# Kernel optimization log

Measured on AMD Instinct MI355X. Metric: run time of the kernel, lower is better.

The kernel has to match this reference:

```python
import jax, jax.numpy as jnp
import numpy as np


def setup_inputs() -> dict:
    key = jax.random.key(0)
    kq, kk, kv = jax.random.split(key, 3)
    N, D = 4096, 1024
    q = jax.random.normal(kq, (N, D), dtype=jnp.float32)
    k = jax.random.normal(kk, (N, D), dtype=jnp.float32)
    v = jax.random.normal(kv, (N, D), dtype=jnp.float32)
    return {"q": q, "k": k, "v": v}


def reference(q, k, v):
    # q, k, v: [N, D]. scale=None, attn_mask unused, dropout p=0.0 (identity).
    scores = jnp.einsum('nd,md->nm', q, k)          # [N, N] logits
    attn = jax.nn.softmax(scores, axis=-1)          # softmax over keys (dim 2 in the [1,N,N] view)
    context = jnp.einsum('nm,md->nd', attn, v)      # [N, D]
    return context
```

## Files before the change

### kernel.cpp

```cpp
#include <hip/hip_runtime.h>
#include <hip/hip_bf16.h>

typedef __attribute__((ext_vector_type(8))) short short8;
typedef __attribute__((ext_vector_type(4))) float float4v;
typedef __attribute__((ext_vector_type(4))) int int4v;

#define L2E 1.44269504088896f
#define SHIFT_C 120.0f
#define QS1 14.0f
#define QS2 3556.0f
#define RATIO 254
#define INV_SS (1.0f / (14.0f * 3556.0f))

#define DRAIN_VM asm volatile("s_waitcnt vmcnt(0)" ::: "memory")
__device__ inline void barrier_raw() {
    asm volatile("" ::: "memory");
    __builtin_amdgcn_s_barrier();
    asm volatile("" ::: "memory");
}

__device__ inline unsigned short f2bf_rne(float x) {
    unsigned int u = __float_as_uint(x);
    u += 0x7FFFu + ((u >> 16) & 1u);
    return (unsigned short)(u >> 16);
}

__device__ inline void gload_lds16(const void* g, void* l) {
    __builtin_amdgcn_global_load_lds(
        (const __attribute__((address_space(1))) void*)g,
        (__attribute__((address_space(3))) void*)l, 16, 0, 0);
}

__global__ __launch_bounds__(256) void prep_fused(
    const float* __restrict__ q, const float* __restrict__ k,
    const float* __restrict__ v,
    signed char* __restrict__ qa, signed char* __restrict__ qb,
    signed char* __restrict__ ka, signed char* __restrict__ kb,
    unsigned short* __restrict__ vt)
{
    __shared__ float tile[32][33];
    int bid = blockIdx.x;
    if (bid < 8192) {
        const size_t n4 = (size_t)4096 * 1024 / 4;
        size_t idx = (size_t)bid * 256 + threadIdx.x;
        const float* src; signed char *da, *db; size_t base;
        if (idx < n4) { src = q; da = qa; db = qb; base = idx; }
        else          { src = k; da = ka; db = kb; base = idx - n4; }
        float4 xv = ((const float4*)src)[base];
        float xs[4] = {xv.x, xv.y, xv.z, xv.w};
        int a[4], b[4];
#pragma unroll
        for (int i = 0; i < 4; ++i) {
            int ia = __float2int_rn(QS1 * xs[i]);
            ia = ia > 127 ? 127 : (ia < -127 ? -127 : ia);
            int ib = __float2int_rn(QS2 * (xs[i] - (float)ia * (1.0f / QS1)));
            ib = ib > 127 ? 127 : (ib < -127 ? -127 : ib);
            a[i] = ia; b[i] = ib;
        }
        unsigned int pa = (a[0] & 255) | ((a[1] & 255) << 8) | ((a[2] & 255) << 16) | ((a[3] & 255) << 24);
        unsigned int pb = (b[0] & 255) | ((b[1] & 255) << 8) | ((b[2] & 255) << 16) | ((b[3] & 255) << 24);
        ((unsigned int*)da)[base] = pa;
        ((unsigned int*)db)[base] = pb;
    } else {
        int b = bid - 8192;
        int k0 = (b & 127) * 32;
        int d0 = (b >> 7) * 32;
        int tx = threadIdx.x & 31, ty = threadIdx.x >> 5;
#pragma unroll
        for (int i = 0; i < 4; ++i) {
            int r = ty + i * 8;
            tile[r][tx] = v[(size_t)(k0 + r) * 1024 + d0 + tx];
        }
        __syncthreads();
#pragma unroll
        for (int i = 0; i < 4; ++i) {
            int r = ty + i * 8;
            vt[(size_t)(d0 + r) * 4096 + k0 + tx] = f2bf_rne(tile[tx][r]);
        }
    }
}

__global__ __launch_bounds__(256) void gemm_qk(
    const signed char* __restrict__ qa, const signed char* __restrict__ qb,
    const signed char* __restrict__ ka, const signed char* __restrict__ kb,
    unsigned short* __restrict__ Pl, float* __restrict__ psum)
{
    __shared__ __align__(16) signed char lds[65536];
    int tid = threadIdx.x;
    int bx = blockIdx.x, by = blockIdx.y;
    int row0 = by * 128, col0 = bx * 128;
    int wave = tid >> 6, lane = tid & 63;
    int wr = (wave >> 1) * 64, wc = (wave & 1) * 64;
    int quad = lane >> 4, lrow = lane & 15;

    int4v acc[4][4];
#pragma unroll
    for (int mi = 0; mi < 4; ++mi)
#pragma unroll
        for (int ni = 0; ni < 4; ++ni) acc[mi][ni] = (int4v){0, 0, 0, 0};

    {
        int sr = lane >> 3, lb = (lane & 7) ^ sr;
        const signed char* gA = qa + (size_t)(row0 + wave * 32 + sr) * 1024 + lb * 16;
        const signed char* gB = ka + (size_t)(col0 + wave * 32 + sr) * 1024 + lb * 16;
        auto stageA = [&](int b, int kc) {
            signed char* lA = lds + b * 32768 + wave * 4096;
            signed char* lB = lds + b * 32768 + 16384 + wave * 4096;
#pragma unroll
            for (int j = 0; j < 4; ++j) {
                gload_lds16(gA + (size_t)j * 8 * 1024 + kc, lA + j * 1024);
                gload_lds16(gB + (size_t)j * 8 * 1024 + kc, lB + j * 1024);
            }
        };
        stageA(0, 0);
        DRAIN_VM; barrier_raw();
        int cur = 0;
        for (int kc = 0; kc < 1024; kc += 128) {
            if (kc + 128 < 1024) stageA(cur ^ 1, kc + 128);
            const signed char* base = lds + cur * 32768;
#pragma unroll
            for (int ks = 0; ks < 2; ++ks) {
                int4v af[4], bf[4];
                int bo = ((ks * 4 + quad) ^ (lrow & 7)) * 16;
#pragma unroll
                for (int mi = 0; mi < 4; ++mi)
                    af[mi] = *(const int4v*)&base[(wr + mi * 16 + lrow) * 128 + bo];
#pragma unroll
                for (int ni = 0; ni < 4; ++ni)
                    bf[ni] = *(const int4v*)&base[16384 + (wc + ni * 16 + lrow) * 128 + bo];
#pragma unroll
                for (int mi = 0; mi < 4; ++mi)
#pragma unroll
                    for (int ni = 0; ni < 4; ++ni)
                        acc[mi][ni] = __builtin_amdgcn_mfma_i32_16x16x64_i8(
                            af[mi], bf[ni], acc[mi][ni], 0, 0, 0);
            }
            DRAIN_VM; barrier_raw();
            cur ^= 1;
        }
    }

#pragma unroll
    for (int mi = 0; mi < 4; ++mi)
#pragma unroll
        for (int ni = 0; ni < 4; ++ni)
#pragma unroll
            for (int r = 0; r < 4; ++r) acc[mi][ni][r] *= RATIO;

    {
        int sr2 = lane >> 2;
        int lb2 = (lane & 3) ^ ((sr2 >> 1) & 3);
        const signed char* gqa = qa + (size_t)(row0 + wave * 32 + sr2) * 1024 + lb2 * 16;
        const signed char* gqb = qb + (size_t)(row0 + wave * 32 + sr2) * 1024 + lb2 * 16;
        const signed char* gka = ka + (size_t)(col0 + wave * 32 + sr2) * 1024 + lb2 * 16;
        const signed char* gkb = kb + (size_t)(col0 + wave * 32 + sr2) * 1024 + lb2 * 16;
        auto stageB = [&](int b, int kc) {
            signed char* base = lds + b * 32768;
#pragma unroll
            for (int j = 0; j < 2; ++j) {
                size_t go = (size_t)j * 16 * 1024 + kc;
                int lo = wave * 2048 + j * 1024;
                gload_lds16(gqa + go, base + lo);
                gload_lds16(gqb + go, base + 8192 + lo);
                gload_lds16(gka + go, base + 16384 + lo);
                gload_lds16(gkb + go, base + 24576 + lo);
            }
        };
        stageB(0, 0);
        DRAIN_VM; barrier_raw();
        int cur = 0;
        for (int kc = 0; kc < 1024; kc += 64) {
            if (kc + 64 < 1024) stageB(cur ^ 1, kc + 64);
            const signed char* base = lds + cur * 32768;
            const signed char* Tqa = base;
            const signed char* Tqb = base + 8192;
            const signed char* Tka = base + 16384;
            const signed char* Tkb = base + 24576;
            int po = (quad ^ ((lrow >> 1) & 3)) * 16;
            {
                int4v fA[4], fB[4];
#pragma unroll
                for (int mi = 0; mi < 4; ++mi)
                    fA[mi] = *(const int4v*)&Tqa[(wr + mi * 16 + lrow) * 64 + po];
#pragma unroll
                for (int ni = 0; ni < 4; ++ni)
                    fB[ni] = *(const int4v*)&Tkb[(wc + ni * 16 + lrow) * 64 + po];
#pragma unroll
                for (int mi = 0; mi < 4; ++mi)
#pragma unroll
                    for (int ni = 0; ni < 4; ++ni)
                        acc[mi][ni] = __builtin_amdgcn_mfma_i32_16x16x64_i8(
                            fA[mi], fB[ni], acc[mi][ni], 0, 0, 0);
            }
            {
                int4v fA[4], fB[4];
#pragma unroll
                for (int mi = 0; mi < 4; ++mi)
                    fA[mi] = *(const int4v*)&Tqb[(wr + mi * 16 + lrow) * 64 + po];
#pragma unroll
                for (int ni = 0; ni < 4; ++ni)
                    fB[ni] = *(const int4v*)&Tka[(wc + ni * 16 + lrow) * 64 + po];
#pragma unroll
                for (int mi = 0; mi < 4; ++mi)
#pragma unroll
                    for (int ni = 0; ni < 4; ++ni)
                        acc[mi][ni] = __builtin_amdgcn_mfma_i32_16x16x64_i8(
                            fA[mi], fB[ni], acc[mi][ni], 0, 0, 0);
            }
            DRAIN_VM; barrier_raw();
            cur ^= 1;
        }
    }

    int strip = bx * 2 + (wave & 1);
#pragma unroll
    for (int mi = 0; mi < 4; ++mi)
#pragma unroll
        for (int r = 0; r < 4; ++r) {
            int row = row0 + wr + mi * 16 + quad * 4 + r;
            float p[4], s = 0.f;
#pragma unroll
            for (int ni = 0; ni < 4; ++ni) {
                float sv = (float)acc[mi][ni][r] * INV_SS;
                p[ni] = exp2f((sv - SHIFT_C) * L2E);
                s += p[ni];
            }
#pragma unroll
            for (int d = 1; d < 16; d <<= 1) s += __shfl_xor(s, d);
#pragma unroll
            for (int ni = 0; ni < 4; ++ni)
                Pl[(size_t)row * 4096 + col0 + wc + ni * 16 + lrow] = f2bf_rne(p[ni]);
            if (lrow == 0) psum[row * 64 + strip] = s;
        }
}

__global__ __launch_bounds__(256) void gemm_pv(
    const unsigned short* __restrict__ P, const unsigned short* __restrict__ vt,
    float* __restrict__ part)
{
    __shared__ __align__(16) unsigned short Ls[32768];
    int tid = threadIdx.x;
    int bx = blockIdx.x, by = blockIdx.y;
    int row0 = by * 128, col0 = bx * 128;
    int kc0 = blockIdx.z * 2048;
    int wave = tid >> 6, lane = tid & 63;
    int wr = (wave >> 1) * 64, wc = (wave & 1) * 64;
    int quad = lane >> 4, lrow = lane & 15;
    int sr = lane >> 3, lb = (lane & 7) ^ sr;
    int swz = lrow & 7;

    float4v acc[4][4];
#pragma unroll
    for (int mi = 0; mi < 4; ++mi)
#pragma unroll
        for (int ni = 0; ni < 4; ++ni) acc[mi][ni] = (float4v){0.f, 0.f, 0.f, 0.f};

    const unsigned short* gA = P  + (size_t)(row0 + wave * 32 + sr) * 4096 + kc0 + lb * 8;
    const unsigned short* gB = vt + (size_t)(col0 + wave * 32 + sr) * 4096 + kc0 + lb * 8;

    auto stage = [&](int b, int kc) {
        unsigned short* lA = Ls + b * 16384 + wave * 2048;
        unsigned short* lB = Ls + b * 16384 + 8192 + wave * 2048;
#pragma unroll
        for (int j = 0; j < 4; ++j) {
            gload_lds16(gA + (size_t)j * 8 * 4096 + kc, lA + j * 512);
            gload_lds16(gB + (size_t)j * 8 * 4096 + kc, lB + j * 512);
        }
    };

    stage(0, 0);
    DRAIN_VM; barrier_raw();
    int cur = 0;
    for (int kc = 0; kc < 2048; kc += 64) {
        if (kc + 64 < 2048) stage(cur ^ 1, kc + 64);
        const unsigned short* As = Ls + cur * 16384;
        const unsigned short* Bs = As + 8192;
#pragma unroll
        for (int ks = 0; ks < 2; ++ks) {
            short8 af[4], bf[4];
            int bo = ((ks * 4 + quad) ^ swz) * 8;
#pragma unroll
            for (int mi = 0; mi < 4; ++mi)
                af[mi] = *(const short8*)&As[(wr + mi * 16 + lrow) * 64 + bo];
#pragma unroll
            for (int ni = 0; ni < 4; ++ni)
                bf[ni] = *(const short8*)&Bs[(wc + ni * 16 + lrow) * 64 + bo];
#pragma unroll
            for (int mi = 0; mi < 4; ++mi)
#pragma unroll
                for (int ni = 0; ni < 4; ++ni)
                    acc[mi][ni] = __builtin_amdgcn_mfma_f32_16x16x32_bf16(
                        af[mi], bf[ni], acc[mi][ni], 0, 0, 0);
        }
        DRAIN_VM; barrier_raw();
        cur ^= 1;
    }
    float* po = part + (size_t)blockIdx.z * 4096 * 1024;
#pragma unroll
    for (int mi = 0; mi < 4; ++mi)
#pragma unroll
        for (int ni = 0; ni < 4; ++ni)
#pragma unroll
            for (int r = 0; r < 4; ++r) {
                int row = row0 + wr + mi * 16 + quad * 4 + r;
                int col = col0 + wc + ni * 16 + lrow;
                po[(size_t)row * 1024 + col] = acc[mi][ni][r];
            }
}

__global__ __launch_bounds__(256) void reduce_out(
    const float* __restrict__ part, const float* __restrict__ psum,
    float* __restrict__ out)
{
    __shared__ float rs;
    int row = blockIdx.x;
    int tid = threadIdx.x;
    if (tid < 64) {
        float s = psum[row * 64 + tid];
#pragma unroll
        for (int d = 1; d < 64; d <<= 1) s += __shfl_xor(s, d);
        if (tid == 0) rs = 1.0f / s;
    }
    __syncthreads();
    float rinv = rs;
    size_t idx = (size_t)row * 256 + tid;
    const float4* p0 = (const float4*)part;
    const float4* p1 = (const float4*)(part + (size_t)4096 * 1024);
    float4 a = p0[idx], b = p1[idx];
    float4 o = {(a.x + b.x) * rinv, (a.y + b.y) * rinv,
                (a.z + b.z) * rinv, (a.w + b.w) * rinv};
    ((float4*)out)[idx] = o;
}

__global__ __launch_bounds__(256) void attn_fallback(
    const float* __restrict__ q, const float* __restrict__ k,
    const float* __restrict__ v, float* __restrict__ out)
{
    __shared__ float qs[1024];
    __shared__ float ps[4096];
    __shared__ float red[256];
    int row = blockIdx.x, tid = threadIdx.x;
    for (int i = tid; i < 1024; i += 256) qs[i] = q[(size_t)row * 1024 + i];
    __syncthreads();
    for (int j = tid; j < 4096; j += 256) {
        const float* kr = &k[(size_t)j * 1024];
        float s = 0.f;
        for (int d = 0; d < 1024; ++d) s += qs[d] * kr[d];
        ps[j] = s;
    }
    __syncthreads();
    float m = -3.4e38f;
    for (int j = tid; j < 4096; j += 256) m = fmaxf(m, ps[j]);
    red[tid] = m; __syncthreads();
    for (int s2 = 128; s2 > 0; s2 >>= 1) {
        if (tid < s2) red[tid] = fmaxf(red[tid], red[tid + s2]);
        __syncthreads();
    }
    m = red[0]; __syncthreads();
    float l = 0.f;
    for (int j = tid; j < 4096; j += 256) {
        float p = exp2f((ps[j] - m) * L2E);
        ps[j] = p; l += p;
    }
    red[tid] = l; __syncthreads();
    for (int s2 = 128; s2 > 0; s2 >>= 1) {
        if (tid < s2) red[tid] += red[tid + s2];
        __syncthreads();
    }
    float rinv = 1.0f / red[0];
    __syncthreads();
    for (int c = tid; c < 1024; c += 256) {
        float o = 0.f;
        for (int j = 0; j < 4096; ++j) o += ps[j] * v[(size_t)j * 1024 + c];
        out[(size_t)row * 1024 + c] = o * rinv;
    }
}

extern "C" void kernel_launch(void* const* d_in, const int* in_sizes, int n_in,
                              void* d_out, int out_size, void* d_ws, size_t ws_size,
                              hipStream_t stream) {
    const float* q = (const float*)d_in[0];
    const float* k = (const float*)d_in[1];
    const float* v = (const float*)d_in[2];
    float* out = (float*)d_out;

    const size_t SZ_P = (size_t)4096 * 4096 * 2;
    const size_t SZ_I = (size_t)4096 * 1024;
    const size_t SZ_H = (size_t)4096 * 1024 * 2;
    const size_t SZ_T = (size_t)4096 * 64 * 4;
    const size_t SZ_PR = (size_t)4096 * 1024 * 4 * 2;
    size_t off = 0;
    char* ws = (char*)d_ws;
    unsigned short* Pbuf = (unsigned short*)(ws + off); off += SZ_P;
    signed char*    qa   = (signed char*)(ws + off);    off += SZ_I;
    signed char*    qb   = (signed char*)(ws + off);    off += SZ_I;
    signed char*    ka   = (signed char*)(ws + off);    off += SZ_I;
    signed char*    kb   = (signed char*)(ws + off);    off += SZ_I;
    unsigned short* vt   = (unsigned short*)(ws + off); off += SZ_H;
    float*          psum = (float*)(ws + off);          off += SZ_T;
    float*          part = (float*)(ws + off);          off += SZ_PR;

    if (ws_size < off) {
        attn_fallback<<<4096, 256, 0, stream>>>(q, k, v, out);
        return;
    }

    prep_fused<<<12288, 256, 0, stream>>>(q, k, v, qa, qb, ka, kb, vt);
    gemm_qk<<<dim3(32, 32), 256, 0, stream>>>(qa, qb, ka, kb, Pbuf, psum);
    gemm_pv<<<dim3(8, 32, 2), 256, 0, stream>>>(Pbuf, vt, part);
    reduce_out<<<4096, 256, 0, stream>>>(part, psum, out);
}
```

Baseline: 210.5 us.

## Fuse hi and cross int8 GEMM passes into one K loop with two accumulators

The two separate K sweeps over Q/K (the high-part GEMM, then the cross-term GEMM) are merged into a single double-buffered loop. It keeps separate high and low int32 accumulators and combines them as hi*RATIO+lo in the epilogue. This removes the second pass of global loads for qa/ka and one full K-loop's barriers. In exchange it doubles accumulator registers, which the added launch_bounds(256,2) may force into spills or limit occupancy.

```diff
diff --git a/kernel.cpp b/kernel.cpp
--- a/kernel.cpp
+++ b/kernel.cpp
@@ -80,7 +80,7 @@
     }
 }
 
-__global__ __launch_bounds__(256) void gemm_qk(
+__global__ __launch_bounds__(256, 2) void gemm_qk(
     const signed char* __restrict__ qa, const signed char* __restrict__ qb,
     const signed char* __restrict__ ka, const signed char* __restrict__ kb,
     unsigned short* __restrict__ Pl, float* __restrict__ psum)
@@ -93,123 +93,81 @@
     int wr = (wave >> 1) * 64, wc = (wave & 1) * 64;
     int quad = lane >> 4, lrow = lane & 15;
 
-    int4v acc[4][4];
+    int4v acch[4][4], accl[4][4];
 #pragma unroll
     for (int mi = 0; mi < 4; ++mi)
 #pragma unroll
-        for (int ni = 0; ni < 4; ++ni) acc[mi][ni] = (int4v){0, 0, 0, 0};
-
-    {
-        int sr = lane >> 3, lb = (lane & 7) ^ sr;
-        const signed char* gA = qa + (size_t)(row0 + wave * 32 + sr) * 1024 + lb * 16;
-        const signed char* gB = ka + (size_t)(col0 + wave * 32 + sr) * 1024 + lb * 16;
-        auto stageA = [&](int b, int kc) {
-            signed char* lA = lds + b * 32768 + wave * 4096;
-            signed char* lB = lds + b * 32768 + 16384 + wave * 4096;
-#pragma unroll
-            for (int j = 0; j < 4; ++j) {
-                gload_lds16(gA + (size_t)j * 8 * 1024 + kc, lA + j * 1024);
-                gload_lds16(gB + (size_t)j * 8 * 1024 + kc, lB + j * 1024);
-            }
-        };
-        stageA(0, 0);
+        for (int ni = 0; ni < 4; ++ni) {
+            acch[mi][ni] = (int4v){0, 0, 0, 0};
+            accl[mi][ni] = (int4v){0, 0, 0, 0};
+        }
+
+    int sr2 = lane >> 2;
+    int lb2 = (lane & 3) ^ ((sr2 >> 1) & 3);
+    const signed char* gqa = qa + (size_t)(row0 + wave * 32 + sr2) * 1024 + lb2 * 16;
+    const signed char* gqb = qb + (size_t)(row0 + wave * 32 + sr2) * 1024 + lb2 * 16;
+    const signed char* gka = ka + (size_t)(col0 + wave * 32 + sr2) * 1024 + lb2 * 16;
+    const signed char* gkb = kb + (size_t)(col0 + wave * 32 + sr2) * 1024 + lb2 * 16;
+
+    auto stage = [&](int b, int kc) {
+        signed char* base = lds + b * 32768;
+#pragma unroll
+        for (int j = 0; j < 2; ++j) {
+            size_t go = (size_t)j * 16 * 1024 + kc;
+            int lo = wave * 2048 + j * 1024;
+            gload_lds16(gqa + go, base + lo);
+            gload_lds16(gqb + go, base + 8192 + lo);
+            gload_lds16(gka + go, base + 16384 + lo);
+            gload_lds16(gkb + go, base + 24576 + lo);
+        }
+    };
+
+    stage(0, 0);
+    DRAIN_VM; barrier_raw();
+    int cur = 0;
+    for (int kc = 0; kc < 1024; kc += 64) {
+        if (kc + 64 < 1024) stage(cur ^ 1, kc + 64);
+        const signed char* base = lds + cur * 32768;
+        const signed char* Tqa = base;
+        const signed char* Tqb = base + 8192;
+        const signed char* Tka = base + 16384;
+        const signed char* Tkb = base + 24576;
+        int po = (quad ^ ((lrow >> 1) & 3)) * 16;
+
+        int4v fqa[4], fka[4], ftmp[4];
+#pragma unroll
+        for (int mi = 0; mi < 4; ++mi)
+            fqa[mi] = *(const int4v*)&Tqa[(wr + mi * 16 + lrow) * 64 + po];
+#pragma unroll
+        for (int ni = 0; ni < 4; ++ni)
+            fka[ni] = *(const int4v*)&Tka[(wc + ni * 16 + lrow) * 64 + po];
+#pragma unroll
+        for (int mi = 0; mi < 4; ++mi)
+#pragma unroll
+            for (int ni = 0; ni < 4; ++ni)
+                acch[mi][ni] = __builtin_amdgcn_mfma_i32_16x16x64_i8(
+                    fqa[mi], fka[ni], acch[mi][ni], 0, 0, 0);
+#pragma unroll
+        for (int ni = 0; ni < 4; ++ni)
+            ftmp[ni] = *(const int4v*)&Tkb[(wc + ni * 16 + lrow) * 64 + po];
+#pragma unroll
+        for (int mi = 0; mi < 4; ++mi)
+#pragma unroll
+            for (int ni = 0; ni < 4; ++ni)
+                accl[mi][ni] = __builtin_amdgcn_mfma_i32_16x16x64_i8(
+                    fqa[mi], ftmp[ni], accl[mi][ni], 0, 0, 0);
+#pragma unroll
+        for (int mi = 0; mi < 4; ++mi)
+            ftmp[mi] = *(const int4v*)&Tqb[(wr + mi * 16 + lrow) * 64 + po];
+#pragma unroll
+        for (int mi = 0; mi < 4; ++mi)
+#pragma unroll
+            for (int ni = 0; ni < 4; ++ni)
+                accl[mi][ni] = __builtin_amdgcn_mfma_i32_16x16x64_i8(
+                    ftmp[mi], fka[ni], accl[mi][ni], 0, 0, 0);
+
         DRAIN_VM; barrier_raw();
-        int cur = 0;
-        for (int kc = 0; kc < 1024; kc += 128) {
-            if (kc + 128 < 1024) stageA(cur ^ 1, kc + 128);
-            const signed char* base = lds + cur * 32768;
-#pragma unroll
-            for (int ks = 0; ks < 2; ++ks) {
-                int4v af[4], bf[4];
-                int bo = ((ks * 4 + quad) ^ (lrow & 7)) * 16;
-#pragma unroll
-                for (int mi = 0; mi < 4; ++mi)
-                    af[mi] = *(const int4v*)&base[(wr + mi * 16 + lrow) * 128 + bo];
-#pragma unroll
-                for (int ni = 0; ni < 4; ++ni)
-                    bf[ni] = *(const int4v*)&base[16384 + (wc + ni * 16 + lrow) * 128 + bo];
-#pragma unroll
-                for (int mi = 0; mi < 4; ++mi)
-#pragma unroll
-                    for (int ni = 0; ni < 4; ++ni)
-                        acc[mi][ni] = __builtin_amdgcn_mfma_i32_16x16x64_i8(
-                            af[mi], bf[ni], acc[mi][ni], 0, 0, 0);
-            }
-            DRAIN_VM; barrier_raw();
-            cur ^= 1;
-        }
-    }
-
-#pragma unroll
-    for (int mi = 0; mi < 4; ++mi)
-#pragma unroll
-        for (int ni = 0; ni < 4; ++ni)
-#pragma unroll
-            for (int r = 0; r < 4; ++r) acc[mi][ni][r] *= RATIO;
-
-    {
-        int sr2 = lane >> 2;
-        int lb2 = (lane & 3) ^ ((sr2 >> 1) & 3);
-        const signed char* gqa = qa + (size_t)(row0 + wave * 32 + sr2) * 1024 + lb2 * 16;
-        const signed char* gqb = qb + (size_t)(row0 + wave * 32 + sr2) * 1024 + lb2 * 16;
-        const signed char* gka = ka + (size_t)(col0 + wave * 32 + sr2) * 1024 + lb2 * 16;
-        const signed char* gkb = kb + (size_t)(col0 + wave * 32 + sr2) * 1024 + lb2 * 16;
-        auto stageB = [&](int b, int kc) {
-            signed char* base = lds + b * 32768;
-#pragma unroll
-            for (int j = 0; j < 2; ++j) {
-                size_t go = (size_t)j * 16 * 1024 + kc;
-                int lo = wave * 2048 + j * 1024;
-                gload_lds16(gqa + go, base + lo);
-                gload_lds16(gqb + go, base + 8192 + lo);
-                gload_lds16(gka + go, base + 16384 + lo);
-                gload_lds16(gkb + go, base + 24576 + lo);
-            }
-        };
-        stageB(0, 0);
-        DRAIN_VM; barrier_raw();
-        int cur = 0;
-        for (int kc = 0; kc < 1024; kc += 64) {
-            if (kc + 64 < 1024) stageB(cur ^ 1, kc + 64);
-            const signed char* base = lds + cur * 32768;
-            const signed char* Tqa = base;
-            const signed char* Tqb = base + 8192;
-            const signed char* Tka = base + 16384;
-            const signed char* Tkb = base + 24576;
-            int po = (quad ^ ((lrow >> 1) & 3)) * 16;
-            {
-                int4v fA[4], fB[4];
-#pragma unroll
-                for (int mi = 0; mi < 4; ++mi)
-                    fA[mi] = *(const int4v*)&Tqa[(wr + mi * 16 + lrow) * 64 + po];
-#pragma unroll
-                for (int ni = 0; ni < 4; ++ni)
-                    fB[ni] = *(const int4v*)&Tkb[(wc + ni * 16 + lrow) * 64 + po];
-#pragma unroll
-                for (int mi = 0; mi < 4; ++mi)
-#pragma unroll
-                    for (int ni = 0; ni < 4; ++ni)
-                        acc[mi][ni] = __builtin_amdgcn_mfma_i32_16x16x64_i8(
-                            fA[mi], fB[ni], acc[mi][ni], 0, 0, 0);
-            }
-            {
-                int4v fA[4], fB[4];
-#pragma unroll
-                for (int mi = 0; mi < 4; ++mi)
-                    fA[mi] = *(const int4v*)&Tqb[(wr + mi * 16 + lrow) * 64 + po];
-#pragma unroll
-                for (int ni = 0; ni < 4; ++ni)
-                    fB[ni] = *(const int4v*)&Tka[(wc + ni * 16 + lrow) * 64 + po];
-#pragma unroll
-                for (int mi = 0; mi < 4; ++mi)
-#pragma unroll
-                    for (int ni = 0; ni < 4; ++ni)
-                        acc[mi][ni] = __builtin_amdgcn_mfma_i32_16x16x64_i8(
-                            fA[mi], fB[ni], acc[mi][ni], 0, 0, 0);
-            }
-            DRAIN_VM; barrier_raw();
-            cur ^= 1;
-        }
+        cur ^= 1;
     }
 
     int strip = bx * 2 + (wave & 1);
@@ -221,7 +179,8 @@
             float p[4], s = 0.f;
 #pragma unroll
             for (int ni = 0; ni < 4; ++ni) {
-                float sv = (float)acc[mi][ni][r] * INV_SS;
+                int s32 = acch[mi][ni][r] * RATIO + accl[mi][ni][r];
+                float sv = (float)s32 * INV_SS;
                 p[ni] = exp2f((sv - SHIFT_C) * L2E);
                 s += p[ni];
             }
```

Measured after the change: 198.1 us. 5.9% less time.
